# Kernel optimization log

Hardware: AMD Instinct MI355X
Metric: run time of the kernel (lower is better)

## Reference

```python
import jax, jax.numpy as jnp
import numpy as np

NODES = 512
SCALE_S, SCALE_M, SCALE_L = 512, 1024, 2048
BATCH = 16
SEQ = SCALE_S + SCALE_M + SCALE_L
EPS = 1e-5


def setup_inputs() -> dict:
    key = jax.random.key(0)
    ks = jax.random.split(key, 10)
    sd = 1.0 / np.sqrt(NODES)
    inp = {
        "x": jax.random.normal(ks[0], (BATCH, SEQ, NODES), dtype=jnp.float32),
        "gamma": jnp.ones((NODES,), jnp.float32),
        "beta": jnp.zeros((NODES,), jnp.float32),
        "Wqkv_s": jax.random.normal(ks[1], (NODES, 3 * NODES), jnp.float32) * sd,
        "bqkv_s": jnp.zeros((3 * NODES,), jnp.float32),
        "Wqkv_m": jax.random.normal(ks[2], (NODES, 3 * NODES), jnp.float32) * sd,
        "bqkv_m": jnp.zeros((3 * NODES,), jnp.float32),
        "Wqkv_l": jax.random.normal(ks[3], (NODES, 3 * NODES), jnp.float32) * sd,
        "bqkv_l": jnp.zeros((3 * NODES,), jnp.float32),
        "Wout": jax.random.normal(ks[4], (NODES, NODES), jnp.float32) * sd,
        "bout": jnp.zeros((NODES,), jnp.float32),
    }
    return inp


def _attn_block(x, W, b, scaling):
    # x: [B, L, N]; fused QKV projection then single-head attention
    qkv = jnp.einsum("bln,nm->blm", x, W) + b
    q, k, v = jnp.split(qkv, 3, axis=-1)
    scores = jnp.einsum("bqn,bkn->bqk", q, k) * scaling
    attn = jax.nn.softmax(scores, axis=-1)
    return jnp.einsum("bqk,bkn->bqn", attn, v)


def reference(x, gamma, beta, Wqkv_s, bqkv_s, Wqkv_m, bqkv_m, Wqkv_l, bqkv_l, Wout, bout):
    res = x
    mu = jnp.mean(x, axis=-1, keepdims=True)
    var = jnp.mean(jnp.square(x - mu), axis=-1, keepdims=True)
    h = (x - mu) * jax.lax.rsqrt(var + EPS) * gamma + beta

    scaling = NODES ** (-0.5)
    xs = h[:, :SCALE_S, :]
    xm = h[:, SCALE_S:SCALE_S + SCALE_M, :]
    xl = h[:, SCALE_S + SCALE_M:SCALE_S + SCALE_M + SCALE_L, :]

    out_s = _attn_block(xs, Wqkv_s, bqkv_s, scaling)
    out_m = _attn_block(xm, Wqkv_m, bqkv_m, scaling)
    out_l = _attn_block(xl, Wqkv_l, bqkv_l, scaling)

    out = jnp.concatenate([out_s, out_m, out_l], axis=1)
    out = jnp.einsum("bln,nm->blm", out, Wout) + bout
    return out + res
```

## Files before the change

kernel.cpp:

```cpp
#include <hip/hip_runtime.h>
#include <stdint.h>

typedef __bf16 bf16;
typedef __bf16 bf16x8 __attribute__((ext_vector_type(8)));
typedef __bf16 bf16x4 __attribute__((ext_vector_type(4)));
typedef float f32x4 __attribute__((ext_vector_type(4)));

#define MFMA16(a, b, c) __builtin_amdgcn_mfma_f32_16x16x32_bf16(a, b, c, 0, 0, 0)

typedef const __attribute__((address_space(1))) uint32_t* gas_t;
typedef __attribute__((address_space(3))) uint32_t* las_t;

__device__ __forceinline__ void gload16(const void* g, void* l) {
  __builtin_amdgcn_global_load_lds((gas_t)g, (las_t)l, 16, 0, 0);
}

__device__ __forceinline__ void stage_tile(const bf16* __restrict__ A, int lda,
                                           const bf16* __restrict__ Bt, int ldb,
                                           int m0, int n0, int k0, bf16* Ad,
                                           bf16* Bd, int w, int r8, int cs) {
#pragma unroll
  for (int i = 0; i < 4; ++i) {
    const int ii = (w << 2) + i;
    const int row = (ii << 3) + r8;
    gload16(A + (size_t)(m0 + row) * lda + k0 + (cs << 3), Ad + (ii << 9));
    gload16(Bt + (size_t)(n0 + row) * ldb + k0 + (cs << 3), Bd + (ii << 9));
  }
}

__device__ __forceinline__ void compute_tile(const bf16* As, const bf16* Bs,
                                             f32x4 (*acc)[4], int lane, int wm,
                                             int wn) {
#pragma unroll
  for (int kk = 0; kk < 2; ++kk) {
    bf16x8 af[4], bfr[4];
#pragma unroll
    for (int mi = 0; mi < 4; ++mi) {
      const int r = wm * 64 + mi * 16 + (lane & 15);
      const int ch = kk * 4 + (lane >> 4);
      af[mi] = *(const bf16x8*)((const char*)As + r * 128 + ((ch ^ (r & 7)) << 4));
    }
#pragma unroll
    for (int ni = 0; ni < 4; ++ni) {
      const int r = wn * 64 + ni * 16 + (lane & 15);
      const int ch = kk * 4 + (lane >> 4);
      bfr[ni] = *(const bf16x8*)((const char*)Bs + r * 128 + ((ch ^ (r & 7)) << 4));
    }
#pragma unroll
    for (int mi = 0; mi < 4; ++mi)
#pragma unroll
      for (int ni = 0; ni < 4; ++ni)
        acc[mi][ni] = MFMA16(af[mi], bfr[ni], acc[mi][ni]);
  }
}

__device__ __forceinline__ void gemm_core(const bf16* __restrict__ A, int lda,
                                          const bf16* __restrict__ Bt, int ldb,
                                          int nk, int m0, int n0,
                                          bf16 (*smem)[128 * 64],
                                          f32x4 (*acc)[4]) {
  const int t = threadIdx.x;
  const int lane = t & 63, w = t >> 6;
  const int wm = w >> 1, wn = w & 1;
  const int r8 = lane >> 3;
  const int cs = (lane & 7) ^ r8;

  stage_tile(A, lda, Bt, ldb, m0, n0, 0, smem[0], smem[2], w, r8, cs);
  __syncthreads();
  int cur = 0;
  for (int kt = 0; kt < nk; ++kt) {
    if (kt + 1 < nk)
      stage_tile(A, lda, Bt, ldb, m0, n0, (kt + 1) << 6, smem[cur ^ 1],
                 smem[2 + (cur ^ 1)], w, r8, cs);
    compute_tile(smem[cur], smem[2 + cur], acc, lane, wm, wn);
    __syncthreads();
    cur ^= 1;
  }
}

__device__ __forceinline__ void epi_put(float* lds, const f32x4* accmi,
                                        int lane, int wm, int wn) {
#pragma unroll
  for (int ni = 0; ni < 4; ++ni) {
    const int c = wn * 64 + ni * 16 + (lane & 15);
    const int lr0 = wm * 16 + ((lane >> 4) << 2);
#pragma unroll
    for (int r = 0; r < 4; ++r) {
      const int lr = lr0 + r;
      lds[(lr << 7) + ((((c >> 2) ^ (lr & 7)) << 2) | (c & 3))] = accmi[ni][r];
    }
  }
}

__device__ __forceinline__ void epi_get(const float* lds, int t, f32x4* v) {
  const int lr = t >> 3, ch0 = (t & 7) << 2;
#pragma unroll
  for (int j = 0; j < 4; ++j)
    v[j] = *(const f32x4*)(lds + (lr << 7) + (((ch0 + j) ^ (lr & 7)) << 2));
}

__global__ __launch_bounds__(256) void transpose_all(
    const float* __restrict__ Ws, const float* __restrict__ Wm,
    const float* __restrict__ Wl, const float* __restrict__ Wo,
    bf16* __restrict__ os, bf16* __restrict__ om, bf16* __restrict__ ol,
    bf16* __restrict__ oo) {
  __shared__ float tile[32][33];
  const int id = blockIdx.x;
  const float* in;
  bf16* outp;
  int N, bx;
  if (id < 768) { in = Ws; outp = os; N = 1536; bx = id; }
  else if (id < 1536) { in = Wm; outp = om; N = 1536; bx = id - 768; }
  else if (id < 2304) { in = Wl; outp = ol; N = 1536; bx = id - 1536; }
  else { in = Wo; outp = oo; N = 512; bx = id - 2304; }
  const int nbx = N >> 5;
  const int n0 = (bx % nbx) * 32, k0 = (bx / nbx) * 32;
  const int tx = threadIdx.x, ty = threadIdx.y;
#pragma unroll
  for (int i = 0; i < 4; ++i)
    tile[ty * 4 + i][tx] = in[(size_t)(k0 + ty * 4 + i) * N + n0 + tx];
  __syncthreads();
#pragma unroll
  for (int i = 0; i < 4; ++i)
    outp[(size_t)(n0 + ty * 4 + i) * 512 + k0 + tx] = (bf16)tile[tx][ty * 4 + i];
}

__global__ __launch_bounds__(256) void ln_kernel(const float* __restrict__ x,
                                                 const float* __restrict__ gamma,
                                                 const float* __restrict__ beta,
                                                 bf16* __restrict__ h) {
  const int t = threadIdx.x, lane = t & 63, w = t >> 6;
  const int row = blockIdx.x * 4 + w;
  const float* xr = x + (size_t)row * 512 + lane * 8;
  float4 v0 = *(const float4*)xr;
  float4 v1 = *(const float4*)(xr + 4);
  float s = v0.x + v0.y + v0.z + v0.w + v1.x + v1.y + v1.z + v1.w;
  float q = v0.x * v0.x + v0.y * v0.y + v0.z * v0.z + v0.w * v0.w +
            v1.x * v1.x + v1.y * v1.y + v1.z * v1.z + v1.w * v1.w;
#pragma unroll
  for (int off = 1; off < 64; off <<= 1) {
    s += __shfl_xor(s, off);
    q += __shfl_xor(q, off);
  }
  const float mean = s * (1.0f / 512.0f);
  const float var = q * (1.0f / 512.0f) - mean * mean;
  const float rs = rsqrtf(var + 1e-5f);
  float4 g0 = *(const float4*)(gamma + lane * 8);
  float4 g1 = *(const float4*)(gamma + lane * 8 + 4);
  float4 b0 = *(const float4*)(beta + lane * 8);
  float4 b1 = *(const float4*)(beta + lane * 8 + 4);
  const int bb = row / 3584;
  const int sp = row - bb * 3584;
  size_t drow;
  if (sp < 512)
    drow = (size_t)bb * 512 + sp;
  else if (sp < 1536)
    drow = 8192 + (size_t)bb * 1024 + (sp - 512);
  else
    drow = 24576 + (size_t)bb * 2048 + (sp - 1536);
  bf16x8 ov = {(bf16)((v0.x - mean) * rs * g0.x + b0.x),
               (bf16)((v0.y - mean) * rs * g0.y + b0.y),
               (bf16)((v0.z - mean) * rs * g0.z + b0.z),
               (bf16)((v0.w - mean) * rs * g0.w + b0.w),
               (bf16)((v1.x - mean) * rs * g1.x + b1.x),
               (bf16)((v1.y - mean) * rs * g1.y + b1.y),
               (bf16)((v1.z - mean) * rs * g1.z + b1.z),
               (bf16)((v1.w - mean) * rs * g1.w + b1.w)};
  *(bf16x8*)(h + drow * 512 + lane * 8) = ov;
}

__global__ __launch_bounds__(256) void qkv_gemm(const bf16* __restrict__ A,
                                                const bf16* __restrict__ Bt,
                                                const float* __restrict__ bias,
                                                bf16* __restrict__ qk,
                                                bf16* __restrict__ vt, int l2L,
                                                int nblk) {
  __shared__ bf16 smem[4][128 * 64];
  const int t = threadIdx.x, lane = t & 63, w = t >> 6;
  const int wm = w >> 1, wn = w & 1;
  const int lg = (blockIdx.x & 7) * (nblk >> 3) + (blockIdx.x >> 3);
  const int m0 = (lg / 12) << 7;
  const int n0 = (lg % 12) << 7;
  const int L = 1 << l2L;

  f32x4 acc[4][4];
#pragma unroll
  for (int i = 0; i < 4; ++i)
#pragma unroll
    for (int j = 0; j < 4; ++j) acc[i][j] = (f32x4)0.0f;

  gemm_core(A, 512, Bt, 512, 8, m0, n0, smem, acc);

  if (n0 < 1024) {
    float* et = (float*)smem;
#pragma unroll
    for (int mi = 0; mi < 4; ++mi) epi_put(et + (mi << 12), acc[mi], lane, wm, wn);
    __syncthreads();
    const int lr = t >> 3, c0l = (t & 7) << 4;
    const int gcol = n0 + c0l;
#pragma unroll
    for (int mi = 0; mi < 4; ++mi) {
      f32x4 v[4];
      epi_get(et + (mi << 12), t, v);
      const int grow = m0 + ((lr >> 4) << 6) + mi * 16 + (lr & 15);
      bf16x8 o0, o1;
#pragma unroll
      for (int j = 0; j < 4; ++j) {
        float4 bv = *(const float4*)(bias + gcol + j * 4);
#pragma unroll
        for (int k = 0; k < 4; ++k) {
          const bf16 val = (bf16)(v[j][k] + ((const float*)&bv)[k]);
          if (j < 2) o0[j * 4 + k] = val;
          else o1[(j - 2) * 4 + k] = val;
        }
      }
      bf16* dst = qk + (size_t)grow * 1024 + gcol;
      *(bf16x8*)dst = o0;
      *(bf16x8*)(dst + 8) = o1;
    }
  } else {
#pragma unroll
    for (int ni = 0; ni < 4; ++ni) {
      const int col = n0 + wn * 64 + ni * 16 + (lane & 15);
      const float bv = bias[col];
#pragma unroll
      for (int mi = 0; mi < 4; ++mi) {
        const int rb = m0 + wm * 64 + mi * 16 + ((lane >> 4) << 2);
        const int d = col - 1024;
        const int bi = rb >> l2L;
        const int kv = rb & (L - 1);
        bf16x4 pk = {(bf16)(acc[mi][ni][0] + bv), (bf16)(acc[mi][ni][1] + bv),
                     (bf16)(acc[mi][ni][2] + bv), (bf16)(acc[mi][ni][3] + bv)};
        *(bf16x4*)(vt + ((size_t)bi * 512 + d) * L + kv) = pk;
      }
    }
  }
}

__global__ __launch_bounds__(256) void sgemm(const bf16* __restrict__ qk,
                                             bf16* __restrict__ sbuf, int l2L,
                                             int b0, float scale, int nblk) {
  __shared__ bf16 smem[4][128 * 64];
  const int t = threadIdx.x, lane = t & 63, w = t >> 6;
  const int wm = w >> 1, wn = w & 1;
  const int L = 1 << l2L;
  const int l2nt = l2L - 7;
  const int lg = (blockIdx.x & 7) * (nblk >> 3) + (blockIdx.x >> 3);
  const int bi = lg >> (2 * l2nt);
  const int rem = lg & ((1 << (2 * l2nt)) - 1);
  const int m0 = (rem >> l2nt) << 7;
  const int n0 = (rem & ((1 << l2nt) - 1)) << 7;

  const bf16* Ab = qk + (size_t)(b0 + bi) * L * 1024;
  const bf16* Bb = Ab + 512;
  bf16* C = sbuf + (size_t)bi * L * L;

  f32x4 acc[4][4];
#pragma unroll
  for (int i = 0; i < 4; ++i)
#pragma unroll
    for (int j = 0; j < 4; ++j) acc[i][j] = (f32x4)0.0f;

  gemm_core(Ab, 1024, Bb, 1024, 8, m0, n0, smem, acc);

  float* et = (float*)smem;
#pragma unroll
  for (int mi = 0; mi < 4; ++mi) epi_put(et + (mi << 12), acc[mi], lane, wm, wn);
  __syncthreads();
  const int lr = t >> 3, c0l = (t & 7) << 4;
#pragma unroll
  for (int mi = 0; mi < 4; ++mi) {
    f32x4 v[4];
    epi_get(et + (mi << 12), t, v);
    const int grow = m0 + ((lr >> 4) << 6) + mi * 16 + (lr & 15);
    bf16x8 o0, o1;
#pragma unroll
    for (int j = 0; j < 4; ++j)
#pragma unroll
      for (int k = 0; k < 4; ++k) {
        const bf16 val = (bf16)(v[j][k] * scale);
        if (j < 2) o0[j * 4 + k] = val;
        else o1[(j - 2) * 4 + k] = val;
      }
    bf16* dst = C + (size_t)grow * L + n0 + c0l;
    *(bf16x8*)dst = o0;
    *(bf16x8*)(dst + 8) = o1;
  }
}

template <int NV>
__global__ __launch_bounds__(256) void softmax_rows(bf16* __restrict__ S) {
  const int t = threadIdx.x, lane = t & 63, w = t >> 6;
  bf16* r = S + ((size_t)blockIdx.x * 4 + w) * (NV * 64);
  bf16x8 raw[NV / 8];
  float f[NV];
#pragma unroll
  for (int i = 0; i < NV / 8; ++i)
    raw[i] = *(const bf16x8*)(r + (i * 64 + lane) * 8);
  float m = -INFINITY;
#pragma unroll
  for (int i = 0; i < NV / 8; ++i)
#pragma unroll
    for (int j = 0; j < 8; ++j) {
      f[i * 8 + j] = (float)raw[i][j];
      m = fmaxf(m, f[i * 8 + j]);
    }
#pragma unroll
  for (int off = 1; off < 64; off <<= 1) m = fmaxf(m, __shfl_xor(m, off));
  const float L2E = 1.44269504088896f;
  float s = 0.0f;
#pragma unroll
  for (int i = 0; i < NV; ++i) {
    f[i] = exp2f((f[i] - m) * L2E);
    s += f[i];
  }
#pragma unroll
  for (int off = 1; off < 64; off <<= 1) s += __shfl_xor(s, off);
  const float inv = 1.0f / s;
#pragma unroll
  for (int i = 0; i < NV / 8; ++i) {
    bf16x8 o;
#pragma unroll
    for (int j = 0; j < 8; ++j) o[j] = (bf16)(f[i * 8 + j] * inv);
    *(bf16x8*)(r + (i * 64 + lane) * 8) = o;
  }
}

__global__ __launch_bounds__(256) void pvgemm(const bf16* __restrict__ sbuf,
                                              const bf16* __restrict__ vt,
                                              bf16* __restrict__ o, int l2L,
                                              int b0, int nblk) {
  __shared__ bf16 smem[4][128 * 64];
  const int t = threadIdx.x, lane = t & 63, w = t >> 6;
  const int wm = w >> 1, wn = w & 1;
  const int L = 1 << l2L;
  const int l2nt = l2L - 7;
  const int lg = (blockIdx.x & 7) * (nblk >> 3) + (blockIdx.x >> 3);
  const int bi = lg >> (l2nt + 2);
  const int rem = lg & ((1 << (l2nt + 2)) - 1);
  const int m0 = (rem >> 2) << 7;
  const int n0 = (rem & 3) << 7;
  const int b = b0 + bi;

  const bf16* Ab = sbuf + (size_t)bi * L * L;
  const bf16* Bb = vt + (size_t)b * 512 * L;
  bf16* C = o + (size_t)b * L * 512;

  f32x4 acc[4][4];
#pragma unroll
  for (int i = 0; i < 4; ++i)
#pragma unroll
    for (int j = 0; j < 4; ++j) acc[i][j] = (f32x4)0.0f;

  gemm_core(Ab, L, Bb, L, L >> 6, m0, n0, smem, acc);

  float* et = (float*)smem;
#pragma unroll
  for (int mi = 0; mi < 4; ++mi) epi_put(et + (mi << 12), acc[mi], lane, wm, wn);
  __syncthreads();
  const int lr = t >> 3, c0l = (t & 7) << 4;
#pragma unroll
  for (int mi = 0; mi < 4; ++mi) {
    f32x4 v[4];
    epi_get(et + (mi << 12), t, v);
    const int grow = m0 + ((lr >> 4) << 6) + mi * 16 + (lr & 15);
    bf16x8 o0, o1;
#pragma unroll
    for (int j = 0; j < 4; ++j)
#pragma unroll
      for (int k = 0; k < 4; ++k) {
        const bf16 val = (bf16)v[j][k];
        if (j < 2) o0[j * 4 + k] = val;
        else o1[(j - 2) * 4 + k] = val;
      }
    bf16* dst = C + (size_t)grow * 512 + n0 + c0l;
    *(bf16x8*)dst = o0;
    *(bf16x8*)(dst + 8) = o1;
  }
}

__device__ __forceinline__ int row2g(int row) {
  if (row < 8192) return ((row >> 9) * 3584) + (row & 511);
  if (row < 24576) {
    const int r = row - 8192;
    return ((r >> 10) * 3584) + 512 + (r & 1023);
  }
  const int r = row - 24576;
  return ((r >> 11) * 3584) + 1536 + (r & 2047);
}

__global__ __launch_bounds__(256) void out_gemm(const bf16* __restrict__ A,
                                                const bf16* __restrict__ Bt,
                                                const float* __restrict__ bias,
                                                const float* __restrict__ x,
                                                float* __restrict__ out) {
  __shared__ bf16 smem[4][128 * 64];
  const int t = threadIdx.x, lane = t & 63, w = t >> 6;
  const int wm = w >> 1, wn = w & 1;
  const int lg = (blockIdx.x & 7) * 224 + (blockIdx.x >> 3);
  const int m0 = (lg >> 2) << 7;
  const int n0 = (lg & 3) << 7;

  f32x4 acc[4][4];
#pragma unroll
  for (int i = 0; i < 4; ++i)
#pragma unroll
    for (int j = 0; j < 4; ++j) acc[i][j] = (f32x4)0.0f;

  gemm_core(A, 512, Bt, 512, 8, m0, n0, smem, acc);

  float* et = (float*)smem;
#pragma unroll
  for (int mi = 0; mi < 4; ++mi) epi_put(et + (mi << 12), acc[mi], lane, wm, wn);
  __syncthreads();
  const int lr = t >> 3, c0l = (t & 7) << 4;
  const int gcol = n0 + c0l;
#pragma unroll
  for (int mi = 0; mi < 4; ++mi) {
    f32x4 v[4];
    epi_get(et + (mi << 12), t, v);
    const int grow = m0 + ((lr >> 4) << 6) + mi * 16 + (lr & 15);
    const int g = row2g(grow);
    const float* xs = x + (size_t)g * 512 + gcol;
    float* os = out + (size_t)g * 512 + gcol;
#pragma unroll
    for (int j = 0; j < 4; ++j) {
      float4 bv = *(const float4*)(bias + gcol + j * 4);
      float4 xv = *(const float4*)(xs + j * 4);
      float4 ov;
      ov.x = v[j][0] + bv.x + xv.x;
      ov.y = v[j][1] + bv.y + xv.y;
      ov.z = v[j][2] + bv.z + xv.z;
      ov.w = v[j][3] + bv.w + xv.w;
      *(float4*)(os + j * 4) = ov;
    }
  }
}

extern "C" void kernel_launch(void* const* d_in, const int* in_sizes, int n_in,
                              void* d_out, int out_size, void* d_ws,
                              size_t ws_size, hipStream_t stream) {
  const float* x = (const float*)d_in[0];
  const float* gamma = (const float*)d_in[1];
  const float* beta = (const float*)d_in[2];
  const float* Wq_s = (const float*)d_in[3];
  const float* bq_s = (const float*)d_in[4];
  const float* Wq_m = (const float*)d_in[5];
  const float* bq_m = (const float*)d_in[6];
  const float* Wq_l = (const float*)d_in[7];
  const float* bq_l = (const float*)d_in[8];
  const float* Wout = (const float*)d_in[9];
  const float* bout = (const float*)d_in[10];
  float* out = (float*)d_out;

  char* ws = (char*)d_ws;
  bf16* h = (bf16*)(ws);
  bf16* qk = (bf16*)(ws + 58720256ull);
  bf16* vt = (bf16*)(ws + 176160768ull);
  bf16* wt_s = (bf16*)(ws + 234881024ull);
  bf16* wt_m = (bf16*)(ws + 236453888ull);
  bf16* wt_l = (bf16*)(ws + 238026752ull);
  bf16* wt_o = (bf16*)(ws + 239599616ull);
  bf16* sbuf = (bf16*)d_out;

  transpose_all<<<2560, dim3(32, 8), 0, stream>>>(Wq_s, Wq_m, Wq_l, Wout, wt_s,
                                                  wt_m, wt_l, wt_o);

  ln_kernel<<<14336, 256, 0, stream>>>(x, gamma, beta, h);

  qkv_gemm<<<768, 256, 0, stream>>>(h, wt_s, bq_s, qk, vt, 9, 768);
  qkv_gemm<<<1536, 256, 0, stream>>>(h + 8192ull * 512, wt_m, bq_m,
                                     qk + 8192ull * 1024, vt + 4194304ull, 10,
                                     1536);
  qkv_gemm<<<3072, 256, 0, stream>>>(h + 24576ull * 512, wt_l, bq_l,
                                     qk + 24576ull * 1024, vt + 12582912ull,
                                     11, 3072);

  const float scale = 0.04419417382415922f;

  sgemm<<<256, 256, 0, stream>>>(qk, sbuf, 9, 0, scale, 256);
  softmax_rows<8><<<2048, 256, 0, stream>>>(sbuf);
  pvgemm<<<256, 256, 0, stream>>>(sbuf, vt, h, 9, 0, 256);

  sgemm<<<1024, 256, 0, stream>>>(qk + 8192ull * 1024, sbuf, 10, 0, scale,
                                  1024);
  softmax_rows<16><<<4096, 256, 0, stream>>>(sbuf);
  pvgemm<<<512, 256, 0, stream>>>(sbuf, vt + 4194304ull, h + 8192ull * 512, 10,
                                  0, 512);

  for (int b0 = 0; b0 < 16; b0 += 8) {
    sgemm<<<2048, 256, 0, stream>>>(qk + 24576ull * 1024, sbuf, 11, b0, scale,
                                    2048);
    softmax_rows<32><<<4096, 256, 0, stream>>>(sbuf);
    pvgemm<<<512, 256, 0, stream>>>(sbuf, vt + 12582912ull, h + 24576ull * 512,
                                    11, b0, 512);
  }

  out_gemm<<<1792, 256, 0, stream>>>(h, wt_o, bout, x, out);
}
```

Measured before the change: 618.1 us.

## Move QKV, score and PV GEMMs to 256x256 tiles with 512-thread blocks

Adds a 256x256 GEMM core with 8 waves per block and double-buffered 64-wide K stages, plus a swizzled two-pass epilogue. The QKV projection, QK^T and PV kernels switch to it, quartering block counts and raising arithmetic intensity per loaded tile. Separately, out_gemm now loads its residual and bias before the main loop so that latency overlaps the GEMM. The risks are fewer blocks (only 64 for the small-scale launches, which underfills the CUs), 128 KB of LDS per block, and higher register pressure from the 8x4 accumulator array.

```diff
diff --git a/kernel.cpp b/kernel.cpp
--- a/kernel.cpp
+++ b/kernel.cpp
@@ -13,6 +13,124 @@
 
 __device__ __forceinline__ void gload16(const void* g, void* l) {
   __builtin_amdgcn_global_load_lds((gas_t)g, (las_t)l, 16, 0, 0);
+}
+
+__device__ __forceinline__ void stage256(const bf16* __restrict__ A, int lda,
+                                         const bf16* __restrict__ Bt, int ldb,
+                                         int m0, int n0, int k0, bf16* Ad,
+                                         bf16* Bd, int w, int r8, int cs) {
+#pragma unroll
+  for (int i = 0; i < 4; ++i) {
+    const int ii = (w << 2) + i;
+    const int row = (ii << 3) + r8;
+    gload16(A + (size_t)(m0 + row) * lda + k0 + (cs << 3), Ad + (ii << 9));
+    gload16(Bt + (size_t)(n0 + row) * ldb + k0 + (cs << 3), Bd + (ii << 9));
+  }
+}
+
+__device__ __forceinline__ void compute256(const bf16* As, const bf16* Bs,
+                                           f32x4 (*acc)[4], int lane, int wm,
+                                           int wn) {
+#pragma unroll
+  for (int kk = 0; kk < 2; ++kk) {
+    bf16x8 bfr[4];
+#pragma unroll
+    for (int ni = 0; ni < 4; ++ni) {
+      const int r = wn * 64 + ni * 16 + (lane & 15);
+      const int ch = kk * 4 + (lane >> 4);
+      bfr[ni] = *(const bf16x8*)((const char*)Bs + r * 128 + ((ch ^ (r & 7)) << 4));
+    }
+#pragma unroll
+    for (int mi = 0; mi < 8; ++mi) {
+      const int r = wm * 128 + mi * 16 + (lane & 15);
+      const int ch = kk * 4 + (lane >> 4);
+      bf16x8 af = *(const bf16x8*)((const char*)As + r * 128 + ((ch ^ (r & 7)) << 4));
+#pragma unroll
+      for (int ni = 0; ni < 4; ++ni)
+        acc[mi][ni] = MFMA16(af, bfr[ni], acc[mi][ni]);
+    }
+  }
+}
+
+__device__ __forceinline__ void gemm256_core(const bf16* __restrict__ A, int lda,
+                                             const bf16* __restrict__ Bt, int ldb,
+                                             int nk, int m0, int n0, bf16* smem,
+                                             f32x4 (*acc)[4]) {
+  const int t = threadIdx.x;
+  const int lane = t & 63, w = t >> 6;
+  const int wm = w >> 2, wn = w & 3;
+  const int r8 = lane >> 3;
+  const int cs = (lane & 7) ^ r8;
+  bf16* Abuf[2] = {smem, smem + 16384};
+  bf16* Bbuf[2] = {smem + 32768, smem + 49152};
+
+  stage256(A, lda, Bt, ldb, m0, n0, 0, Abuf[0], Bbuf[0], w, r8, cs);
+  for (int kt = 0; kt < nk; ++kt) {
+    const int cur = kt & 1;
+    if (kt + 1 < nk) {
+      stage256(A, lda, Bt, ldb, m0, n0, (kt + 1) << 6, Abuf[cur ^ 1],
+               Bbuf[cur ^ 1], w, r8, cs);
+      asm volatile("s_waitcnt vmcnt(8)" ::: "memory");
+    } else {
+      asm volatile("s_waitcnt vmcnt(0)" ::: "memory");
+    }
+    __builtin_amdgcn_s_barrier();
+    __builtin_amdgcn_sched_barrier(0);
+    __builtin_amdgcn_s_setprio(1);
+    compute256(Abuf[cur], Bbuf[cur], acc, lane, wm, wn);
+    __builtin_amdgcn_s_setprio(0);
+    __builtin_amdgcn_s_barrier();
+  }
+}
+
+__device__ __forceinline__ void epi256_bf16(float* et, f32x4 (*acc)[4],
+                                            bf16* dst, int ldc, int m0, int n0,
+                                            const float* bias, float scale,
+                                            int t, int lane, int wm, int wn) {
+  const int lrr = t >> 2, cb = (t & 3) << 4;
+#pragma unroll
+  for (int h = 0; h < 2; ++h) {
+    __syncthreads();
+#pragma unroll
+    for (int q = 0; q < 4; ++q) {
+#pragma unroll
+      for (int ni = 0; ni < 4; ++ni) {
+        const int c = wn * 64 + ni * 16 + (lane & 15);
+        const int lr0 = wm * 64 + q * 16 + ((lane >> 4) << 2);
+#pragma unroll
+        for (int r = 0; r < 4; ++r) {
+          const int lr = lr0 + r;
+          et[lr * 256 + (((c >> 2) ^ (lr & 7)) << 2) + (c & 3)] =
+              acc[h * 4 + q][ni][r];
+        }
+      }
+    }
+    __syncthreads();
+    const int grow = m0 + ((lrr >> 6) << 7) + h * 64 + (lrr & 63);
+    const int gcb = n0 + ((t & 3) << 6);
+    bf16* drow = dst + (size_t)grow * ldc + gcb;
+#pragma unroll
+    for (int k = 0; k < 8; ++k) {
+      f32x4 v0 = *(const f32x4*)(et + lrr * 256 + (((cb + 2 * k) ^ (lrr & 7)) << 2));
+      f32x4 v1 = *(const f32x4*)(et + lrr * 256 + (((cb + 2 * k + 1) ^ (lrr & 7)) << 2));
+      bf16x8 o;
+      if (bias) {
+        float4 b0 = *(const float4*)(bias + gcb + k * 8);
+        float4 b1 = *(const float4*)(bias + gcb + k * 8 + 4);
+        o[0] = (bf16)(v0[0] + b0.x); o[1] = (bf16)(v0[1] + b0.y);
+        o[2] = (bf16)(v0[2] + b0.z); o[3] = (bf16)(v0[3] + b0.w);
+        o[4] = (bf16)(v1[0] + b1.x); o[5] = (bf16)(v1[1] + b1.y);
+        o[6] = (bf16)(v1[2] + b1.z); o[7] = (bf16)(v1[3] + b1.w);
+      } else {
+#pragma unroll
+        for (int i = 0; i < 4; ++i) {
+          o[i] = (bf16)(v0[i] * scale);
+          o[4 + i] = (bf16)(v1[i] * scale);
+        }
+      }
+      *(bf16x8*)(drow + k * 8) = o;
+    }
+  }
 }
 
 __device__ __forceinline__ void stage_tile(const bf16* __restrict__ A, int lda,
@@ -169,64 +287,40 @@
   *(bf16x8*)(h + drow * 512 + lane * 8) = ov;
 }
 
-__global__ __launch_bounds__(256) void qkv_gemm(const bf16* __restrict__ A,
-                                                const bf16* __restrict__ Bt,
-                                                const float* __restrict__ bias,
-                                                bf16* __restrict__ qk,
-                                                bf16* __restrict__ vt, int l2L,
-                                                int nblk) {
-  __shared__ bf16 smem[4][128 * 64];
+__global__ __launch_bounds__(512, 2) void qkv_gemm(const bf16* __restrict__ A,
+                                                   const bf16* __restrict__ Bt,
+                                                   const float* __restrict__ bias,
+                                                   bf16* __restrict__ qk,
+                                                   bf16* __restrict__ vt,
+                                                   int l2L, int nblk) {
+  __shared__ bf16 smem[4][256 * 64];
   const int t = threadIdx.x, lane = t & 63, w = t >> 6;
-  const int wm = w >> 1, wn = w & 1;
+  const int wm = w >> 2, wn = w & 3;
   const int lg = (blockIdx.x & 7) * (nblk >> 3) + (blockIdx.x >> 3);
-  const int m0 = (lg / 12) << 7;
-  const int n0 = (lg % 12) << 7;
+  const int m0 = (lg / 6) << 8;
+  const int nt = lg % 6;
+  const int n0 = nt << 8;
   const int L = 1 << l2L;
 
-  f32x4 acc[4][4];
-#pragma unroll
-  for (int i = 0; i < 4; ++i)
+  f32x4 acc[8][4];
+#pragma unroll
+  for (int i = 0; i < 8; ++i)
 #pragma unroll
     for (int j = 0; j < 4; ++j) acc[i][j] = (f32x4)0.0f;
 
-  gemm_core(A, 512, Bt, 512, 8, m0, n0, smem, acc);
-
-  if (n0 < 1024) {
-    float* et = (float*)smem;
-#pragma unroll
-    for (int mi = 0; mi < 4; ++mi) epi_put(et + (mi << 12), acc[mi], lane, wm, wn);
-    __syncthreads();
-    const int lr = t >> 3, c0l = (t & 7) << 4;
-    const int gcol = n0 + c0l;
-#pragma unroll
-    for (int mi = 0; mi < 4; ++mi) {
-      f32x4 v[4];
-      epi_get(et + (mi << 12), t, v);
-      const int grow = m0 + ((lr >> 4) << 6) + mi * 16 + (lr & 15);
-      bf16x8 o0, o1;
-#pragma unroll
-      for (int j = 0; j < 4; ++j) {
-        float4 bv = *(const float4*)(bias + gcol + j * 4);
-#pragma unroll
-        for (int k = 0; k < 4; ++k) {
-          const bf16 val = (bf16)(v[j][k] + ((const float*)&bv)[k]);
-          if (j < 2) o0[j * 4 + k] = val;
-          else o1[(j - 2) * 4 + k] = val;
-        }
-      }
-      bf16* dst = qk + (size_t)grow * 1024 + gcol;
-      *(bf16x8*)dst = o0;
-      *(bf16x8*)(dst + 8) = o1;
-    }
+  gemm256_core(A, 512, Bt, 512, 8, m0, n0, &smem[0][0], acc);
+
+  if (nt < 4) {
+    epi256_bf16((float*)smem, acc, qk, 1024, m0, n0, bias, 1.0f, t, lane, wm, wn);
   } else {
 #pragma unroll
     for (int ni = 0; ni < 4; ++ni) {
       const int col = n0 + wn * 64 + ni * 16 + (lane & 15);
       const float bv = bias[col];
-#pragma unroll
-      for (int mi = 0; mi < 4; ++mi) {
-        const int rb = m0 + wm * 64 + mi * 16 + ((lane >> 4) << 2);
-        const int d = col - 1024;
+      const int d = col - 1024;
+#pragma unroll
+      for (int mi = 0; mi < 8; ++mi) {
+        const int rb = m0 + wm * 128 + mi * 16 + ((lane >> 4) << 2);
         const int bi = rb >> l2L;
         const int kv = rb & (L - 1);
         bf16x4 pk = {(bf16)(acc[mi][ni][0] + bv), (bf16)(acc[mi][ni][1] + bv),
@@ -237,55 +331,33 @@
   }
 }
 
-__global__ __launch_bounds__(256) void sgemm(const bf16* __restrict__ qk,
-                                             bf16* __restrict__ sbuf, int l2L,
-                                             int b0, float scale, int nblk) {
-  __shared__ bf16 smem[4][128 * 64];
+__global__ __launch_bounds__(512, 2) void sgemm(const bf16* __restrict__ qk,
+                                                bf16* __restrict__ sbuf, int l2L,
+                                                int b0, float scale, int nblk) {
+  __shared__ bf16 smem[4][256 * 64];
   const int t = threadIdx.x, lane = t & 63, w = t >> 6;
-  const int wm = w >> 1, wn = w & 1;
+  const int wm = w >> 2, wn = w & 3;
   const int L = 1 << l2L;
-  const int l2nt = l2L - 7;
+  const int l2nt = l2L - 8;
   const int lg = (blockIdx.x & 7) * (nblk >> 3) + (blockIdx.x >> 3);
   const int bi = lg >> (2 * l2nt);
   const int rem = lg & ((1 << (2 * l2nt)) - 1);
-  const int m0 = (rem >> l2nt) << 7;
-  const int n0 = (rem & ((1 << l2nt) - 1)) << 7;
+  const int m0 = (rem >> l2nt) << 8;
+  const int n0 = (rem & ((1 << l2nt) - 1)) << 8;
 
   const bf16* Ab = qk + (size_t)(b0 + bi) * L * 1024;
   const bf16* Bb = Ab + 512;
   bf16* C = sbuf + (size_t)bi * L * L;
 
-  f32x4 acc[4][4];
-#pragma unroll
-  for (int i = 0; i < 4; ++i)
+  f32x4 acc[8][4];
+#pragma unroll
+  for (int i = 0; i < 8; ++i)
 #pragma unroll
     for (int j = 0; j < 4; ++j) acc[i][j] = (f32x4)0.0f;
 
-  gemm_core(Ab, 1024, Bb, 1024, 8, m0, n0, smem, acc);
-
-  float* et = (float*)smem;
-#pragma unroll
-  for (int mi = 0; mi < 4; ++mi) epi_put(et + (mi << 12), acc[mi], lane, wm, wn);
-  __syncthreads();
-  const int lr = t >> 3, c0l = (t & 7) << 4;
-#pragma unroll
-  for (int mi = 0; mi < 4; ++mi) {
-    f32x4 v[4];
-    epi_get(et + (mi << 12), t, v);
-    const int grow = m0 + ((lr >> 4) << 6) + mi * 16 + (lr & 15);
-    bf16x8 o0, o1;
-#pragma unroll
-    for (int j = 0; j < 4; ++j)
-#pragma unroll
-      for (int k = 0; k < 4; ++k) {
-        const bf16 val = (bf16)(v[j][k] * scale);
-        if (j < 2) o0[j * 4 + k] = val;
-        else o1[(j - 2) * 4 + k] = val;
-      }
-    bf16* dst = C + (size_t)grow * L + n0 + c0l;
-    *(bf16x8*)dst = o0;
-    *(bf16x8*)(dst + 8) = o1;
-  }
+  gemm256_core(Ab, 1024, Bb, 1024, 8, m0, n0, &smem[0][0], acc);
+
+  epi256_bf16((float*)smem, acc, C, L, m0, n0, nullptr, scale, t, lane, wm, wn);
 }
 
 template <int NV>
@@ -326,57 +398,35 @@
   }
 }
 
-__global__ __launch_bounds__(256) void pvgemm(const bf16* __restrict__ sbuf,
-                                              const bf16* __restrict__ vt,
-                                              bf16* __restrict__ o, int l2L,
-                                              int b0, int nblk) {
-  __shared__ bf16 smem[4][128 * 64];
+__global__ __launch_bounds__(512, 2) void pvgemm(const bf16* __restrict__ sbuf,
+                                                 const bf16* __restrict__ vt,
+                                                 bf16* __restrict__ o, int l2L,
+                                                 int b0, int nblk) {
+  __shared__ bf16 smem[4][256 * 64];
   const int t = threadIdx.x, lane = t & 63, w = t >> 6;
-  const int wm = w >> 1, wn = w & 1;
+  const int wm = w >> 2, wn = w & 3;
   const int L = 1 << l2L;
-  const int l2nt = l2L - 7;
+  const int l2nt = l2L - 8;
   const int lg = (blockIdx.x & 7) * (nblk >> 3) + (blockIdx.x >> 3);
-  const int bi = lg >> (l2nt + 2);
-  const int rem = lg & ((1 << (l2nt + 2)) - 1);
-  const int m0 = (rem >> 2) << 7;
-  const int n0 = (rem & 3) << 7;
+  const int bi = lg >> (l2nt + 1);
+  const int rem = lg & ((1 << (l2nt + 1)) - 1);
+  const int m0 = (rem >> 1) << 8;
+  const int n0 = (rem & 1) << 8;
   const int b = b0 + bi;
 
   const bf16* Ab = sbuf + (size_t)bi * L * L;
   const bf16* Bb = vt + (size_t)b * 512 * L;
   bf16* C = o + (size_t)b * L * 512;
 
-  f32x4 acc[4][4];
-#pragma unroll
-  for (int i = 0; i < 4; ++i)
+  f32x4 acc[8][4];
+#pragma unroll
+  for (int i = 0; i < 8; ++i)
 #pragma unroll
     for (int j = 0; j < 4; ++j) acc[i][j] = (f32x4)0.0f;
 
-  gemm_core(Ab, L, Bb, L, L >> 6, m0, n0, smem, acc);
-
-  float* et = (float*)smem;
-#pragma unroll
-  for (int mi = 0; mi < 4; ++mi) epi_put(et + (mi << 12), acc[mi], lane, wm, wn);
-  __syncthreads();
-  const int lr = t >> 3, c0l = (t & 7) << 4;
-#pragma unroll
-  for (int mi = 0; mi < 4; ++mi) {
-    f32x4 v[4];
-    epi_get(et + (mi << 12), t, v);
-    const int grow = m0 + ((lr >> 4) << 6) + mi * 16 + (lr & 15);
-    bf16x8 o0, o1;
-#pragma unroll
-    for (int j = 0; j < 4; ++j)
-#pragma unroll
-      for (int k = 0; k < 4; ++k) {
-        const bf16 val = (bf16)v[j][k];
-        if (j < 2) o0[j * 4 + k] = val;
-        else o1[(j - 2) * 4 + k] = val;
-      }
-    bf16* dst = C + (size_t)grow * 512 + n0 + c0l;
-    *(bf16x8*)dst = o0;
-    *(bf16x8*)(dst + 8) = o1;
-  }
+  gemm256_core(Ab, L, Bb, L, L >> 6, m0, n0, &smem[0][0], acc);
+
+  epi256_bf16((float*)smem, acc, C, 512, m0, n0, nullptr, 1.0f, t, lane, wm, wn);
 }
 
 __device__ __forceinline__ int row2g(int row) {
@@ -401,6 +451,22 @@
   const int m0 = (lg >> 2) << 7;
   const int n0 = (lg & 3) << 7;
 
+  const int lr = t >> 3, c0l = (t & 7) << 4;
+  const int gcol = n0 + c0l;
+  int gidx[4];
+  f32x4 xv[4][4];
+  float4 bvv[4];
+#pragma unroll
+  for (int j = 0; j < 4; ++j) bvv[j] = *(const float4*)(bias + gcol + j * 4);
+#pragma unroll
+  for (int mi = 0; mi < 4; ++mi) {
+    const int grow = m0 + ((lr >> 4) << 6) + mi * 16 + (lr & 15);
+    gidx[mi] = row2g(grow);
+#pragma unroll
+    for (int j = 0; j < 4; ++j)
+      xv[mi][j] = *(const f32x4*)(x + (size_t)gidx[mi] * 512 + gcol + j * 4);
+  }
+
   f32x4 acc[4][4];
 #pragma unroll
   for (int i = 0; i < 4; ++i)
@@ -413,25 +479,18 @@
 #pragma unroll
   for (int mi = 0; mi < 4; ++mi) epi_put(et + (mi << 12), acc[mi], lane, wm, wn);
   __syncthreads();
-  const int lr = t >> 3, c0l = (t & 7) << 4;
-  const int gcol = n0 + c0l;
 #pragma unroll
   for (int mi = 0; mi < 4; ++mi) {
     f32x4 v[4];
     epi_get(et + (mi << 12), t, v);
-    const int grow = m0 + ((lr >> 4) << 6) + mi * 16 + (lr & 15);
-    const int g = row2g(grow);
-    const float* xs = x + (size_t)g * 512 + gcol;
-    float* os = out + (size_t)g * 512 + gcol;
+    float* os = out + (size_t)gidx[mi] * 512 + gcol;
 #pragma unroll
     for (int j = 0; j < 4; ++j) {
-      float4 bv = *(const float4*)(bias + gcol + j * 4);
-      float4 xv = *(const float4*)(xs + j * 4);
       float4 ov;
-      ov.x = v[j][0] + bv.x + xv.x;
-      ov.y = v[j][1] + bv.y + xv.y;
-      ov.z = v[j][2] + bv.z + xv.z;
-      ov.w = v[j][3] + bv.w + xv.w;
+      ov.x = v[j][0] + bvv[j].x + xv[mi][j][0];
+      ov.y = v[j][1] + bvv[j].y + xv[mi][j][1];
+      ov.z = v[j][2] + bvv[j].z + xv[mi][j][2];
+      ov.w = v[j][3] + bvv[j].w + xv[mi][j][3];
       *(float4*)(os + j * 4) = ov;
     }
   }
@@ -468,32 +527,31 @@
 
   ln_kernel<<<14336, 256, 0, stream>>>(x, gamma, beta, h);
 
-  qkv_gemm<<<768, 256, 0, stream>>>(h, wt_s, bq_s, qk, vt, 9, 768);
-  qkv_gemm<<<1536, 256, 0, stream>>>(h + 8192ull * 512, wt_m, bq_m,
-                                     qk + 8192ull * 1024, vt + 4194304ull, 10,
-                                     1536);
-  qkv_gemm<<<3072, 256, 0, stream>>>(h + 24576ull * 512, wt_l, bq_l,
-                                     qk + 24576ull * 1024, vt + 12582912ull,
-                                     11, 3072);
+  qkv_gemm<<<192, 512, 0, stream>>>(h, wt_s, bq_s, qk, vt, 9, 192);
+  qkv_gemm<<<384, 512, 0, stream>>>(h + 8192ull * 512, wt_m, bq_m,
+                                    qk + 8192ull * 1024, vt + 4194304ull, 10,
+                                    384);
+  qkv_gemm<<<768, 512, 0, stream>>>(h + 24576ull * 512, wt_l, bq_l,
+                                    qk + 24576ull * 1024, vt + 12582912ull, 11,
+                                    768);
 
   const float scale = 0.04419417382415922f;
 
-  sgemm<<<256, 256, 0, stream>>>(qk, sbuf, 9, 0, scale, 256);
+  sgemm<<<64, 512, 0, stream>>>(qk, sbuf, 9, 0, scale, 64);
   softmax_rows<8><<<2048, 256, 0, stream>>>(sbuf);
-  pvgemm<<<256, 256, 0, stream>>>(sbuf, vt, h, 9, 0, 256);
-
-  sgemm<<<1024, 256, 0, stream>>>(qk + 8192ull * 1024, sbuf, 10, 0, scale,
-                                  1024);
+  pvgemm<<<64, 512, 0, stream>>>(sbuf, vt, h, 9, 0, 64);
+
+  sgemm<<<256, 512, 0, stream>>>(qk + 8192ull * 1024, sbuf, 10, 0, scale, 256);
   softmax_rows<16><<<4096, 256, 0, stream>>>(sbuf);
-  pvgemm<<<512, 256, 0, stream>>>(sbuf, vt + 4194304ull, h + 8192ull * 512, 10,
-                                  0, 512);
+  pvgemm<<<128, 512, 0, stream>>>(sbuf, vt + 4194304ull, h + 8192ull * 512, 10,
+                                  0, 128);
 
   for (int b0 = 0; b0 < 16; b0 += 8) {
-    sgemm<<<2048, 256, 0, stream>>>(qk + 24576ull * 1024, sbuf, 11, b0, scale,
-                                    2048);
+    sgemm<<<512, 512, 0, stream>>>(qk + 24576ull * 1024, sbuf, 11, b0, scale,
+                                   512);
     softmax_rows<32><<<4096, 256, 0, stream>>>(sbuf);
-    pvgemm<<<512, 256, 0, stream>>>(sbuf, vt + 12582912ull, h + 24576ull * 512,
-                                    11, b0, 512);
+    pvgemm<<<128, 512, 0, stream>>>(sbuf, vt + 12582912ull, h + 24576ull * 512,
+                                    11, b0, 128);
   }
 
   out_gemm<<<1792, 256, 0, stream>>>(h, wt_o, bout, x, out);
```

New measurement: 858.4 us. +38.9%, slower.
